# Kernel tuning notes

Hardware: AMD Instinct MI355X
Metric: run time of the kernel (lower is better)

The kernel has to match this reference:

```python
import jax, jax.numpy as jnp
import numpy as np

D, T, B = 128, 64, 512
EPS = 1e-5


def setup_inputs() -> dict:
    key = jax.random.key(0)
    k1, k2, k3, k4, k5 = jax.random.split(key, 5)
    inp = jax.random.normal(k1, (D, T, B), jnp.float32) * 0.1
    returns_partition = jax.random.normal(k2, (D, T, B), jnp.float32) * 0.01
    target = jax.random.normal(k3, (D,), jnp.float32) * 0.1
    hidden = jnp.zeros((D, 1, B), jnp.float32)  # forward arg (overwritten at t=0)
    # diagonally-dominant weight so the per-row denominators v[j,j] stay away from 0
    W = jnp.eye(D, dtype=jnp.float32) + 0.1 * jax.random.normal(k4, (D, D), jnp.float32)
    b = 0.1 * jax.random.normal(k5, (D,), jnp.float32)
    return {"input": inp, "target": target, "returns_partition": returns_partition,
            "hidden": hidden, "W": W, "b": b}


def _recurrence(h, v, absb, pi_bar):
    # h, pi_bar: [D, B]; v: [D, D] (row-normalized); absb: [D]
    d = h.shape[0]
    vd = jnp.diagonal(v)                                  # v[j, j], torch.matmul(vj, e_j)
    s = v @ (h - pi_bar)                                  # [D, B], s[j] = vj . (h - pi_bar)
    lam_p = (absb[:, None] - s) / vd[:, None]
    lam_m = (-absb[:, None] - s) / vd[:, None]
    delta = (jnp.where(s > absb[:, None], lam_p, 0.0)
             + jnp.where(s < -absb[:, None], lam_m, 0.0))  # [D, B]
    # hidden_new_j = h + delta[j] * e_j  =>  v @ (hidden_new_j - pi_bar) = s + v[:, j] (x) delta[j]
    snew = s[None, :, :] + v.T[:, :, None] * delta[:, None, :]      # [J, D, B]
    inside = (snew < absb[None, :, None] + EPS) & (snew > -absb[None, :, None] - EPS)
    # torch: judge_mat[j] = min over rows; then max over j  == any_j(all_k(...))
    judge_mat = jnp.any(jnp.all(inside, axis=1), axis=0).astype(h.dtype)  # [B]

    # sequential per-coordinate projection (order matters: row j uses updated state)
    def body(ht, j):
        sj = v[j] @ (ht - pi_bar)                          # [B]
        lp = (absb[j] - sj) / v[j, j]
        lm = (-absb[j] - sj) / v[j, j]
        dj = jnp.where(sj > absb[j], lp, 0.0) + jnp.where(sj < -absb[j], lm, 0.0)
        return ht.at[j].add(dj), None
    h_temp, _ = jax.lax.scan(body, h, jnp.arange(d))

    # 10-step bisection between pi_bar (feasible) and (1 - judge_mat) * h
    def bis(carry, _):
        h_in, h_out = carry
        h_m = h_in + (h_out - h_in) * 0.5
        sm = v @ (h_m - pi_bar)
        j = jnp.all((sm <= absb[:, None] + EPS) & (sm >= -absb[:, None] - EPS), axis=0)  # [B]
        return (jnp.where(j, h_m, h_in), jnp.where(j, h_out, h_m)), h_m
    h_out0 = (1.0 - judge_mat) * h
    _, h_ms = jax.lax.scan(bis, (pi_bar, h_out0), None, length=10)
    h_m = h_ms[-1]
    return judge_mat * h_temp + (1.0 - judge_mat) * h_m


def reference(input, target, returns_partition, hidden, W, b):
    d, t, bsz = input.shape
    norm = jnp.linalg.norm(W, axis=1, keepdims=True)
    v = W / jnp.maximum(norm, 1e-12)                      # F.normalize(W, p=2, dim=1)
    absb = jnp.abs(b)
    pi_bar = jnp.broadcast_to(target[:, None], (d, bsz))  # [D, B]

    h0 = input[:, 0, :]                                   # t = 0: hidden := input slice
    rs = jnp.moveaxis(returns_partition[:, :t - 1, :], 1, 0)  # [T-1, D, B]

    def step(h, r):
        adj = h * (1.0 + r) / (1.0 + jnp.sum(h * r, axis=0))
        hn = _recurrence(adj, v, absb, pi_bar)
        return hn, hn

    h_last, hs = jax.lax.scan(step, h0, rs)
    output = jnp.concatenate([h0[:, None, :], jnp.moveaxis(hs, 0, 1)], axis=1)  # [D, T, B]
    return output, h_last[:, None, :]
```

## Files before the change

kernel.cpp:

```cpp
#include <hip/hip_runtime.h>
#include <cstdint>

#define D 128
#define T 64
#define B 512
#define EPSF 1e-5f

__device__ __forceinline__ float lane_bcast(float x, int l) {
    return __int_as_float(__builtin_amdgcn_readlane(__float_as_int(x), l));
}

__device__ __forceinline__ float2 colpair(const float* csh, int j, int i2) {
    int f2 = j * 64 + (i2 ^ ((j & 7) << 1));
    return *(const float2*)(csh + 2 * f2);
}

__global__ __launch_bounds__(64) void prep_kernel(const float* __restrict__ W,
                                                  const float* __restrict__ b,
                                                  float* __restrict__ csw,
                                                  float* __restrict__ vd,
                                                  float* __restrict__ absb) {
    const int i = blockIdx.x;
    const int l = threadIdx.x;
    float w0 = W[i * D + l];
    float w1 = W[i * D + l + 64];
    float p = w0 * w0 + w1 * w1;
#pragma unroll
    for (int off = 32; off; off >>= 1) p += __shfl_xor(p, off);
    float norm = sqrtf(p);
    float scale = norm > 1e-12f ? norm : 1e-12f;
    float v0 = w0 / scale;
    float v1 = w1 / scale;
    const int i2 = i & 63, half = i >> 6;
    const int sw = (l & 7) << 1;
    csw[2 * (l * 64 + (i2 ^ sw)) + half] = v0;
    csw[2 * ((l + 64) * 64 + (i2 ^ sw)) + half] = v1;
    if (i < 64) { if (l == i) vd[i] = v0; }
    else        { if (l == i - 64) vd[i] = v1; }
    if (i == 0) {
        absb[l] = fabsf(b[l]);
        absb[l + 64] = fabsf(b[l + 64]);
    }
}

__global__ __launch_bounds__(128) void rnn_kernel(const float* __restrict__ input,
                                                  const float* __restrict__ target,
                                                  const float* __restrict__ returns,
                                                  const float* __restrict__ cswg,
                                                  const float* __restrict__ vdg,
                                                  const float* __restrict__ absbg,
                                                  float* __restrict__ out) {
    __shared__ float csh[D * D];
    __shared__ float s_sh[2][2 * 64];
    __shared__ float ae_sh[2 * 64];

    const int tid = threadIdx.x;
    const int w = tid >> 6;
    const int lane = tid & 63;
    const int b = blockIdx.x * 2 + w;
    const int rlo = lane, rhi = lane + 64;

    {
        const float4* src = (const float4*)cswg;
        float4* dst = (float4*)csh;
#pragma unroll
        for (int c = 0; c < 32; ++c) dst[c * 128 + tid] = src[c * 128 + tid];
    }

    const float tgt_lo = target[rlo], tgt_hi = target[rhi];
    const float a_lo = absbg[rlo], a_hi = absbg[rhi];
    const float aeps_lo = a_lo + EPSF, aeps_hi = a_hi + EPSF;
    const float vd_lo = vdg[rlo], vd_hi = vdg[rhi];
    const float rvd_lo = 1.0f / vd_lo, rvd_hi = 1.0f / vd_hi;

    if (w == 0) *(float2*)&ae_sh[2 * lane] = make_float2(aeps_lo, aeps_hi);
    __syncthreads();

    const char* colp[8];
#pragma unroll
    for (int c = 0; c < 8; ++c)
        colp[c] = (const char*)csh + 8 * (lane ^ (c << 1));

    float h_lo = input[rlo * T * B + b];
    float h_hi = input[rhi * T * B + b];
    out[rlo * T * B + b] = h_lo;
    out[rhi * T * B + b] = h_hi;

    float r_lo = returns[rlo * T * B + b];
    float r_hi = returns[rhi * T * B + b];

    for (int t = 1; t < T; ++t) {
        float num_lo = h_lo * (1.0f + r_lo);
        float num_hi = h_hi * (1.0f + r_hi);
        float p = h_lo * r_lo + h_hi * r_hi;
#pragma unroll
        for (int off = 32; off; off >>= 1) p += __shfl_xor(p, off);
        float den = 1.0f + p;
        float adj_lo = num_lo / den;
        float adj_hi = num_hi / den;

        if (t < T - 1) {
            r_lo = returns[rlo * T * B + t * B + b];
            r_hi = returns[rhi * T * B + t * B + b];
        }

        const float x_lo = adj_lo - tgt_lo;
        const float x_hi = adj_hi - tgt_hi;

        float a0 = 0, a1 = 0, a2 = 0, a3 = 0;
        float b0 = 0, b1 = 0, b2 = 0, b3 = 0;
#pragma unroll
        for (int k = 0; k < 128; ++k) {
            float2 cp = *(const float2*)(colp[k & 7] + k * 512);
            float xk = lane_bcast((k < 64) ? x_lo : x_hi, k & 63);
            switch (k & 3) {
                case 0: a0 = fmaf(cp.x, xk, a0); b0 = fmaf(cp.y, xk, b0); break;
                case 1: a1 = fmaf(cp.x, xk, a1); b1 = fmaf(cp.y, xk, b1); break;
                case 2: a2 = fmaf(cp.x, xk, a2); b2 = fmaf(cp.y, xk, b2); break;
                default: a3 = fmaf(cp.x, xk, a3); b3 = fmaf(cp.y, xk, b3); break;
            }
        }
        float s_lo = (a0 + a1) + (a2 + a3);
        float s_hi = (b0 + b1) + (b2 + b3);

        h_lo = adj_lo;
        h_hi = adj_hi;

        uint64_t mlo = __ballot(fabsf(s_lo) > a_lo);
        uint64_t mhi = __ballot(fabsf(s_hi) > a_hi);

        if ((mlo | mhi) != 0ull) {
            float dl = 0.0f, dh = 0.0f;
            if (s_lo > a_lo) dl = (a_lo - s_lo) / vd_lo;
            else if (s_lo < -a_lo) dl = (-a_lo - s_lo) / vd_lo;
            if (s_hi > a_hi) dh = (a_hi - s_hi) / vd_hi;
            else if (s_hi < -a_hi) dh = (-a_hi - s_hi) / vd_hi;

            int V = __popcll(mlo) + __popcll(mhi);
            bool judge = false;

            if (V <= 8) {
                bool in_lo = (s_lo < aeps_lo) && (s_lo > -aeps_lo);
                bool in_hi = (s_hi < aeps_hi) && (s_hi > -aeps_hi);
                judge = (__ballot(in_lo && in_hi) == ~0ull);
                if (!judge) {
                    uint64_t tml = mlo, tmh = mhi;
                    int jn[8];
                    float djs[8];
                    float2 cps[8];
#pragma unroll
                    for (int q = 0; q < 8; ++q) {
                        int j = -1;
                        if (tml) {
                            j = (int)__ffsll((unsigned long long)tml) - 1;
                            tml &= tml - 1;
                        } else if (tmh) {
                            j = 64 + (int)__ffsll((unsigned long long)tmh) - 1;
                            tmh &= tmh - 1;
                        }
                        jn[q] = j;
                        if (j >= 0) {
                            djs[q] = lane_bcast((j < 64) ? dl : dh, j & 63);
                            cps[q] = colpair(csh, j, lane);
                        }
                    }
#pragma unroll
                    for (int q = 0; q < 8; ++q) {
                        if (jn[q] >= 0 && !judge) {
                            float n_lo = fmaf(cps[q].x, djs[q], s_lo);
                            float n_hi = fmaf(cps[q].y, djs[q], s_hi);
                            bool pl = (n_lo < aeps_lo) && (n_lo > -aeps_lo);
                            bool ph = (n_hi < aeps_hi) && (n_hi > -aeps_hi);
                            if (__ballot(pl && ph) == ~0ull) judge = true;
                        }
                    }
                }
            } else {
                *(float2*)&s_sh[w][2 * lane] = make_float2(s_lo, s_hi);
                float m1 = -1.0f, m2 = -1.0f;
#pragma unroll
                for (int c = 0; c < 32; ++c) {
                    int f4 = lane * 32 + (c ^ (lane & 7));
                    float4 c1 = *(const float4*)(csh + 4 * f4);
                    float4 c2 = *(const float4*)(csh + 4 * f4 + 8192);
                    int i2a = (2 * c) ^ ((lane & 7) << 1);
                    float4 sv = *(const float4*)&s_sh[w][2 * i2a];
                    float4 ae = *(const float4*)&ae_sh[2 * i2a];
                    m1 = fmaxf(m1, fabsf(fmaf(c1.x, dl, sv.x)) - ae.x);
                    m1 = fmaxf(m1, fabsf(fmaf(c1.y, dl, sv.y)) - ae.y);
                    m1 = fmaxf(m1, fabsf(fmaf(c1.z, dl, sv.z)) - ae.z);
                    m1 = fmaxf(m1, fabsf(fmaf(c1.w, dl, sv.w)) - ae.w);
                    m2 = fmaxf(m2, fabsf(fmaf(c2.x, dh, sv.x)) - ae.x);
                    m2 = fmaxf(m2, fabsf(fmaf(c2.y, dh, sv.y)) - ae.y);
                    m2 = fmaxf(m2, fabsf(fmaf(c2.z, dh, sv.z)) - ae.z);
                    m2 = fmaxf(m2, fabsf(fmaf(c2.w, dh, sv.w)) - ae.w);
                }
                judge = ((__ballot(m1 < 0.0f) | __ballot(m2 < 0.0f)) != 0ull);
            }

            if (judge) {
                uint64_t rem_lo = ~0ull, rem_hi = ~0ull;
                while (true) {
                    uint64_t vl = __ballot(fabsf(s_lo) > a_lo) & rem_lo;
                    uint64_t vh = __ballot(fabsf(s_hi) > a_hi) & rem_hi;
                    if (!(vl | vh)) break;
                    int jq[4];
                    float2 cpq[4];
                    {
                        uint64_t tl = vl, th = vh;
#pragma unroll
                        for (int q = 0; q < 4; ++q) {
                            int j = -1;
                            if (tl) {
                                j = (int)__ffsll((unsigned long long)tl) - 1;
                                tl &= tl - 1;
                            } else if (th) {
                                j = 64 + (int)__ffsll((unsigned long long)th) - 1;
                                th &= th - 1;
                            }
                            jq[q] = j;
                            if (j >= 0) cpq[q] = colpair(csh, j, lane);
                        }
                    }
                    bool abort = false;
#pragma unroll
                    for (int q = 0; q < 4; ++q) {
                        if (abort || jq[q] < 0) continue;
                        uint64_t cl = __ballot(fabsf(s_lo) > a_lo) & rem_lo;
                        uint64_t ch = __ballot(fabsf(s_hi) > a_hi) & rem_hi;
                        int jl = cl ? (int)__ffsll((unsigned long long)cl) - 1
                                    : (ch ? 64 + (int)__ffsll((unsigned long long)ch) - 1 : -1);
                        if (jl < 0) { rem_lo = rem_hi = 0ull; abort = true; continue; }
                        if (jl < jq[q]) { abort = true; continue; }
                        if (jl > jq[q]) continue;
                        float tl2 = (s_lo > a_lo) ? (a_lo - s_lo)
                                   : ((s_lo < -a_lo) ? (-a_lo - s_lo) : 0.0f);
                        float th2 = (s_hi > a_hi) ? (a_hi - s_hi)
                                   : ((s_hi < -a_hi) ? (-a_hi - s_hi) : 0.0f);
                        float dj = lane_bcast((jq[q] < 64) ? tl2 * rvd_lo : th2 * rvd_hi,
                                              jq[q] & 63);
                        if (lane == (jq[q] & 63)) {
                            if (jq[q] < 64) h_lo += dj; else h_hi += dj;
                        }
                        s_lo = fmaf(cpq[q].x, dj, s_lo);
                        s_hi = fmaf(cpq[q].y, dj, s_hi);
                        if (jq[q] < 64) {
                            rem_lo = (jq[q] == 63) ? 0ull : (~0ull << (jq[q] + 1));
                        } else {
                            rem_lo = 0ull;
                            int sh = jq[q] - 64;
                            rem_hi = (sh == 63) ? 0ull : (~0ull << (sh + 1));
                        }
                    }
                    if (!(rem_lo | rem_hi)) break;
                }
            } else {
                float hin_lo = tgt_lo, hin_hi = tgt_hi;
                float sin_lo = 0.0f, sin_hi = 0.0f;
                float hout_lo = h_lo, hout_hi = h_hi;
                float sout_lo = s_lo, sout_hi = s_hi;
                float hm_lo = 0.0f, hm_hi = 0.0f;
#pragma unroll
                for (int it = 0; it < 10; ++it) {
                    hm_lo = hin_lo + (hout_lo - hin_lo) * 0.5f;
                    hm_hi = hin_hi + (hout_hi - hin_hi) * 0.5f;
                    float sm_lo = sin_lo + (sout_lo - sin_lo) * 0.5f;
                    float sm_hi = sin_hi + (sout_hi - sin_hi) * 0.5f;
                    bool pl = (sm_lo <= aeps_lo) && (sm_lo >= -aeps_lo);
                    bool ph = (sm_hi <= aeps_hi) && (sm_hi >= -aeps_hi);
                    bool inside = (__ballot(pl && ph) == ~0ull);
                    if (inside) {
                        hin_lo = hm_lo; hin_hi = hm_hi;
                        sin_lo = sm_lo; sin_hi = sm_hi;
                    } else {
                        hout_lo = hm_lo; hout_hi = hm_hi;
                        sout_lo = sm_lo; sout_hi = sm_hi;
                    }
                }
                h_lo = hm_lo;
                h_hi = hm_hi;
            }
        }

        out[rlo * T * B + t * B + b] = h_lo;
        out[rhi * T * B + t * B + b] = h_hi;
    }

    out[D * T * B + rlo * B + b] = h_lo;
    out[D * T * B + rhi * B + b] = h_hi;
}

extern "C" void kernel_launch(void* const* d_in, const int* in_sizes, int n_in,
                              void* d_out, int out_size, void* d_ws, size_t ws_size,
                              hipStream_t stream) {
    const float* input   = (const float*)d_in[0];
    const float* target  = (const float*)d_in[1];
    const float* returns = (const float*)d_in[2];
    const float* W = (const float*)d_in[4];
    const float* b = (const float*)d_in[5];
    float* out = (float*)d_out;

    float* csw  = (float*)d_ws;
    float* vd   = csw + D * D;
    float* absb = vd + D;

    prep_kernel<<<D, 64, 0, stream>>>(W, b, csw, vd, absb);
    rnn_kernel<<<B / 2, 128, 0, stream>>>(input, target, returns, csw, vd, absb, out);
}
```

Measured before the change: 235.5 us.

## Process two batch columns per wavefront to reuse each shared-memory weight load

Each 64-thread block now runs a single wavefront that handles two batch elements instead of one. Every float2 read of the normalized weight matrix from LDS therefore feeds FMAs for both samples, and the x vector is broadcast through LDS float4 reads rather than per-element readlane. Global loads and stores become float2 over the adjacent batch pair. The violation checks, sequential projection and bisection are duplicated per sample and run under shared control flow, so divergent paths may serialize. The block now holds 64KB of LDS for one wavefront, which halves the resident waves per CU.

```diff
diff --git a/kernel.cpp b/kernel.cpp
--- a/kernel.cpp
+++ b/kernel.cpp
@@ -43,28 +43,29 @@
     }
 }
 
-__global__ __launch_bounds__(128) void rnn_kernel(const float* __restrict__ input,
-                                                  const float* __restrict__ target,
-                                                  const float* __restrict__ returns,
-                                                  const float* __restrict__ cswg,
-                                                  const float* __restrict__ vdg,
-                                                  const float* __restrict__ absbg,
-                                                  float* __restrict__ out) {
+__global__ __launch_bounds__(64) void rnn_kernel(const float* __restrict__ input,
+                                                 const float* __restrict__ target,
+                                                 const float* __restrict__ returns,
+                                                 const float* __restrict__ cswg,
+                                                 const float* __restrict__ vdg,
+                                                 const float* __restrict__ absbg,
+                                                 float* __restrict__ out) {
     __shared__ float csh[D * D];
-    __shared__ float s_sh[2][2 * 64];
-    __shared__ float ae_sh[2 * 64];
-
-    const int tid = threadIdx.x;
-    const int w = tid >> 6;
-    const int lane = tid & 63;
-    const int b = blockIdx.x * 2 + w;
+    __shared__ __align__(16) float xsA[128];
+    __shared__ __align__(16) float xsB[128];
+    __shared__ __align__(16) float ssA[128];
+    __shared__ __align__(16) float ssB[128];
+    __shared__ __align__(16) float aes[128];
+
+    const int lane = threadIdx.x;
+    const int bA = blockIdx.x * 2;
     const int rlo = lane, rhi = lane + 64;
 
     {
         const float4* src = (const float4*)cswg;
         float4* dst = (float4*)csh;
 #pragma unroll
-        for (int c = 0; c < 32; ++c) dst[c * 128 + tid] = src[c * 128 + tid];
+        for (int c = 0; c < 64; ++c) dst[c * 64 + lane] = src[c * 64 + lane];
     }
 
     const float tgt_lo = target[rlo], tgt_hi = target[rhi];
@@ -72,222 +73,298 @@
     const float aeps_lo = a_lo + EPSF, aeps_hi = a_hi + EPSF;
     const float vd_lo = vdg[rlo], vd_hi = vdg[rhi];
     const float rvd_lo = 1.0f / vd_lo, rvd_hi = 1.0f / vd_hi;
-
-    if (w == 0) *(float2*)&ae_sh[2 * lane] = make_float2(aeps_lo, aeps_hi);
-    __syncthreads();
-
-    const char* colp[8];
-#pragma unroll
-    for (int c = 0; c < 8; ++c)
-        colp[c] = (const char*)csh + 8 * (lane ^ (c << 1));
-
-    float h_lo = input[rlo * T * B + b];
-    float h_hi = input[rhi * T * B + b];
-    out[rlo * T * B + b] = h_lo;
-    out[rhi * T * B + b] = h_hi;
-
-    float r_lo = returns[rlo * T * B + b];
-    float r_hi = returns[rhi * T * B + b];
+    *(float2*)&aes[2 * lane] = make_float2(aeps_lo, aeps_hi);
+
+    const char* cb[8];
+#pragma unroll
+    for (int c = 0; c < 8; ++c) cb[c] = (const char*)csh + 8 * (lane ^ (c << 1));
+
+    float2 hL = *(const float2*)&input[rlo * T * B + bA];
+    float2 hH = *(const float2*)&input[rhi * T * B + bA];
+    *(float2*)&out[rlo * T * B + bA] = hL;
+    *(float2*)&out[rhi * T * B + bA] = hH;
+    float hA_lo = hL.x, hB_lo = hL.y, hA_hi = hH.x, hB_hi = hH.y;
+
+    float2 r2L = *(const float2*)&returns[rlo * T * B + bA];
+    float2 r2H = *(const float2*)&returns[rhi * T * B + bA];
+    float rA_lo = r2L.x, rB_lo = r2L.y, rA_hi = r2H.x, rB_hi = r2H.y;
 
     for (int t = 1; t < T; ++t) {
-        float num_lo = h_lo * (1.0f + r_lo);
-        float num_hi = h_hi * (1.0f + r_hi);
-        float p = h_lo * r_lo + h_hi * r_hi;
-#pragma unroll
-        for (int off = 32; off; off >>= 1) p += __shfl_xor(p, off);
-        float den = 1.0f + p;
-        float adj_lo = num_lo / den;
-        float adj_hi = num_hi / den;
+        float pA = hA_lo * rA_lo + hA_hi * rA_hi;
+        float pB = hB_lo * rB_lo + hB_hi * rB_hi;
+#pragma unroll
+        for (int off = 32; off; off >>= 1) {
+            pA += __shfl_xor(pA, off);
+            pB += __shfl_xor(pB, off);
+        }
+        float rdA = 1.0f / (1.0f + pA);
+        float rdB = 1.0f / (1.0f + pB);
+        float adjA_lo = hA_lo * (1.0f + rA_lo) * rdA;
+        float adjA_hi = hA_hi * (1.0f + rA_hi) * rdA;
+        float adjB_lo = hB_lo * (1.0f + rB_lo) * rdB;
+        float adjB_hi = hB_hi * (1.0f + rB_hi) * rdB;
 
         if (t < T - 1) {
-            r_lo = returns[rlo * T * B + t * B + b];
-            r_hi = returns[rhi * T * B + t * B + b];
+            r2L = *(const float2*)&returns[rlo * T * B + t * B + bA];
+            r2H = *(const float2*)&returns[rhi * T * B + t * B + bA];
+            rA_lo = r2L.x; rB_lo = r2L.y; rA_hi = r2H.x; rB_hi = r2H.y;
         }
 
-        const float x_lo = adj_lo - tgt_lo;
-        const float x_hi = adj_hi - tgt_hi;
-
-        float a0 = 0, a1 = 0, a2 = 0, a3 = 0;
-        float b0 = 0, b1 = 0, b2 = 0, b3 = 0;
-#pragma unroll
-        for (int k = 0; k < 128; ++k) {
-            float2 cp = *(const float2*)(colp[k & 7] + k * 512);
-            float xk = lane_bcast((k < 64) ? x_lo : x_hi, k & 63);
-            switch (k & 3) {
-                case 0: a0 = fmaf(cp.x, xk, a0); b0 = fmaf(cp.y, xk, b0); break;
-                case 1: a1 = fmaf(cp.x, xk, a1); b1 = fmaf(cp.y, xk, b1); break;
-                case 2: a2 = fmaf(cp.x, xk, a2); b2 = fmaf(cp.y, xk, b2); break;
-                default: a3 = fmaf(cp.x, xk, a3); b3 = fmaf(cp.y, xk, b3); break;
+        float xA_lo = adjA_lo - tgt_lo, xA_hi = adjA_hi - tgt_hi;
+        float xB_lo = adjB_lo - tgt_lo, xB_hi = adjB_hi - tgt_hi;
+        xsA[lane] = xA_lo; xsA[64 + lane] = xA_hi;
+        xsB[lane] = xB_lo; xsB[64 + lane] = xB_hi;
+
+        float aL0 = 0, aL1 = 0, aH0 = 0, aH1 = 0;
+        float bL0 = 0, bL1 = 0, bH0 = 0, bH1 = 0;
+#pragma unroll
+        for (int m = 0; m < 32; ++m) {
+            float4 xA4 = *(const float4*)&xsA[4 * m];
+            float4 xB4 = *(const float4*)&xsB[4 * m];
+#pragma unroll
+            for (int e = 0; e < 4; ++e) {
+                const int k = 4 * m + e;
+                float2 vp = *(const float2*)(cb[k & 7] + k * 512);
+                float xa = (&xA4.x)[e], xb = (&xB4.x)[e];
+                if (e & 1) {
+                    aL1 = fmaf(vp.x, xa, aL1); aH1 = fmaf(vp.y, xa, aH1);
+                    bL1 = fmaf(vp.x, xb, bL1); bH1 = fmaf(vp.y, xb, bH1);
+                } else {
+                    aL0 = fmaf(vp.x, xa, aL0); aH0 = fmaf(vp.y, xa, aH0);
+                    bL0 = fmaf(vp.x, xb, bL0); bH0 = fmaf(vp.y, xb, bH0);
+                }
             }
         }
-        float s_lo = (a0 + a1) + (a2 + a3);
-        float s_hi = (b0 + b1) + (b2 + b3);
-
-        h_lo = adj_lo;
-        h_hi = adj_hi;
-
-        uint64_t mlo = __ballot(fabsf(s_lo) > a_lo);
-        uint64_t mhi = __ballot(fabsf(s_hi) > a_hi);
-
-        if ((mlo | mhi) != 0ull) {
-            float dl = 0.0f, dh = 0.0f;
-            if (s_lo > a_lo) dl = (a_lo - s_lo) / vd_lo;
-            else if (s_lo < -a_lo) dl = (-a_lo - s_lo) / vd_lo;
-            if (s_hi > a_hi) dh = (a_hi - s_hi) / vd_hi;
-            else if (s_hi < -a_hi) dh = (-a_hi - s_hi) / vd_hi;
-
-            int V = __popcll(mlo) + __popcll(mhi);
-            bool judge = false;
-
-            if (V <= 8) {
-                bool in_lo = (s_lo < aeps_lo) && (s_lo > -aeps_lo);
-                bool in_hi = (s_hi < aeps_hi) && (s_hi > -aeps_hi);
-                judge = (__ballot(in_lo && in_hi) == ~0ull);
-                if (!judge) {
-                    uint64_t tml = mlo, tmh = mhi;
-                    int jn[8];
-                    float djs[8];
-                    float2 cps[8];
-#pragma unroll
-                    for (int q = 0; q < 8; ++q) {
-                        int j = -1;
-                        if (tml) {
-                            j = (int)__ffsll((unsigned long long)tml) - 1;
-                            tml &= tml - 1;
-                        } else if (tmh) {
-                            j = 64 + (int)__ffsll((unsigned long long)tmh) - 1;
-                            tmh &= tmh - 1;
+        float sA_lo = aL0 + aL1, sA_hi = aH0 + aH1;
+        float sB_lo = bL0 + bL1, sB_hi = bH0 + bH1;
+
+        hA_lo = adjA_lo; hA_hi = adjA_hi;
+        hB_lo = adjB_lo; hB_hi = adjB_hi;
+
+        uint64_t mAlo = __ballot(fabsf(sA_lo) > a_lo);
+        uint64_t mAhi = __ballot(fabsf(sA_hi) > a_hi);
+        uint64_t mBlo = __ballot(fabsf(sB_lo) > a_lo);
+        uint64_t mBhi = __ballot(fabsf(sB_hi) > a_hi);
+        bool violA = (mAlo | mAhi) != 0ull;
+        bool violB = (mBlo | mBhi) != 0ull;
+
+        if (violA || violB) {
+            bool judgeA = true, judgeB = true;
+            bool needPJA = false, needPJB = false;
+            float dlA = 0, dhA = 0, dlB = 0, dhB = 0;
+
+            if (violA) {
+                if (sA_lo > a_lo) dlA = (a_lo - sA_lo) / vd_lo;
+                else if (sA_lo < -a_lo) dlA = (-a_lo - sA_lo) / vd_lo;
+                if (sA_hi > a_hi) dhA = (a_hi - sA_hi) / vd_hi;
+                else if (sA_hi < -a_hi) dhA = (-a_hi - sA_hi) / vd_hi;
+                int VA = __popcll(mAlo) + __popcll(mAhi);
+                if (VA <= 8) {
+                    bool in0 = (sA_lo < aeps_lo) && (sA_lo > -aeps_lo) &&
+                               (sA_hi < aeps_hi) && (sA_hi > -aeps_hi);
+                    judgeA = (__ballot(in0) == ~0ull);
+                    if (!judgeA) {
+                        uint64_t tml = mAlo, tmh = mAhi;
+                        unsigned bits = 0;
+#pragma unroll
+                        for (int q = 0; q < 8; ++q) {
+                            int j = -1;
+                            if (tml) { j = (int)__ffsll((unsigned long long)tml) - 1; tml &= tml - 1; }
+                            else if (tmh) { j = 64 + (int)__ffsll((unsigned long long)tmh) - 1; tmh &= tmh - 1; }
+                            if (j >= 0) {
+                                float dj = lane_bcast((j < 64) ? dlA : dhA, j & 63);
+                                float2 cp = colpair(csh, j, lane);
+                                float nlo = fmaf(cp.x, dj, sA_lo);
+                                float nhi = fmaf(cp.y, dj, sA_hi);
+                                bool ok = (nlo < aeps_lo) && (nlo > -aeps_lo) &&
+                                          (nhi < aeps_hi) && (nhi > -aeps_hi);
+                                bits |= ok ? (1u << q) : 0u;
+                            }
                         }
-                        jn[q] = j;
-                        if (j >= 0) {
-                            djs[q] = lane_bcast((j < 64) ? dl : dh, j & 63);
-                            cps[q] = colpair(csh, j, lane);
+#pragma unroll
+                        for (int off = 1; off < 64; off <<= 1)
+                            bits &= (unsigned)__shfl_xor((int)bits, off);
+                        judgeA = (bits != 0u);
+                    }
+                } else {
+                    needPJA = true;
+                }
+            }
+            if (violB) {
+                if (sB_lo > a_lo) dlB = (a_lo - sB_lo) / vd_lo;
+                else if (sB_lo < -a_lo) dlB = (-a_lo - sB_lo) / vd_lo;
+                if (sB_hi > a_hi) dhB = (a_hi - sB_hi) / vd_hi;
+                else if (sB_hi < -a_hi) dhB = (-a_hi - sB_hi) / vd_hi;
+                int VB = __popcll(mBlo) + __popcll(mBhi);
+                if (VB <= 8) {
+                    bool in0 = (sB_lo < aeps_lo) && (sB_lo > -aeps_lo) &&
+                               (sB_hi < aeps_hi) && (sB_hi > -aeps_hi);
+                    judgeB = (__ballot(in0) == ~0ull);
+                    if (!judgeB) {
+                        uint64_t tml = mBlo, tmh = mBhi;
+                        unsigned bits = 0;
+#pragma unroll
+                        for (int q = 0; q < 8; ++q) {
+                            int j = -1;
+                            if (tml) { j = (int)__ffsll((unsigned long long)tml) - 1; tml &= tml - 1; }
+                            else if (tmh) { j = 64 + (int)__ffsll((unsigned long long)tmh) - 1; tmh &= tmh - 1; }
+                            if (j >= 0) {
+                                float dj = lane_bcast((j < 64) ? dlB : dhB, j & 63);
+                                float2 cp = colpair(csh, j, lane);
+                                float nlo = fmaf(cp.x, dj, sB_lo);
+                                float nhi = fmaf(cp.y, dj, sB_hi);
+                                bool ok = (nlo < aeps_lo) && (nlo > -aeps_lo) &&
+                                          (nhi < aeps_hi) && (nhi > -aeps_hi);
+                                bits |= ok ? (1u << q) : 0u;
+                            }
                         }
-                    }
-#pragma unroll
-                    for (int q = 0; q < 8; ++q) {
-                        if (jn[q] >= 0 && !judge) {
-                            float n_lo = fmaf(cps[q].x, djs[q], s_lo);
-                            float n_hi = fmaf(cps[q].y, djs[q], s_hi);
-                            bool pl = (n_lo < aeps_lo) && (n_lo > -aeps_lo);
-                            bool ph = (n_hi < aeps_hi) && (n_hi > -aeps_hi);
-                            if (__ballot(pl && ph) == ~0ull) judge = true;
+#pragma unroll
+                        for (int off = 1; off < 64; off <<= 1)
+                            bits &= (unsigned)__shfl_xor((int)bits, off);
+                        judgeB = (bits != 0u);
+                    }
+                } else {
+                    needPJB = true;
+                }
+            }
+
+            if (needPJA || needPJB) {
+                if (needPJA) *(float2*)&ssA[2 * lane] = make_float2(sA_lo, sA_hi);
+                if (needPJB) *(float2*)&ssB[2 * lane] = make_float2(sB_lo, sB_hi);
+                float m1A = -1.0f, m2A = -1.0f, m1B = -1.0f, m2B = -1.0f;
+                const int jx = lane & 7;
+                const float* jbase = csh + 128 * lane;
+#pragma unroll
+                for (int c = 0; c < 32; ++c) {
+                    const float* pr = jbase + 4 * (c ^ jx);
+                    float4 c1 = *(const float4*)pr;
+                    float4 c2 = *(const float4*)(pr + 8192);
+                    float4 ae = *(const float4*)&aes[4 * c];
+                    if (needPJA) {
+                        float4 sv = *(const float4*)&ssA[4 * c];
+                        m1A = fmaxf(m1A, fabsf(fmaf(c1.x, dlA, sv.x)) - ae.x);
+                        m1A = fmaxf(m1A, fabsf(fmaf(c1.y, dlA, sv.y)) - ae.y);
+                        m1A = fmaxf(m1A, fabsf(fmaf(c1.z, dlA, sv.z)) - ae.z);
+                        m1A = fmaxf(m1A, fabsf(fmaf(c1.w, dlA, sv.w)) - ae.w);
+                        m2A = fmaxf(m2A, fabsf(fmaf(c2.x, dhA, sv.x)) - ae.x);
+                        m2A = fmaxf(m2A, fabsf(fmaf(c2.y, dhA, sv.y)) - ae.y);
+                        m2A = fmaxf(m2A, fabsf(fmaf(c2.z, dhA, sv.z)) - ae.z);
+                        m2A = fmaxf(m2A, fabsf(fmaf(c2.w, dhA, sv.w)) - ae.w);
+                    }
+                    if (needPJB) {
+                        float4 sv = *(const float4*)&ssB[4 * c];
+                        m1B = fmaxf(m1B, fabsf(fmaf(c1.x, dlB, sv.x)) - ae.x);
+                        m1B = fmaxf(m1B, fabsf(fmaf(c1.y, dlB, sv.y)) - ae.y);
+                        m1B = fmaxf(m1B, fabsf(fmaf(c1.z, dlB, sv.z)) - ae.z);
+                        m1B = fmaxf(m1B, fabsf(fmaf(c1.w, dlB, sv.w)) - ae.w);
+                        m2B = fmaxf(m2B, fabsf(fmaf(c2.x, dhB, sv.x)) - ae.x);
+                        m2B = fmaxf(m2B, fabsf(fmaf(c2.y, dhB, sv.y)) - ae.y);
+                        m2B = fmaxf(m2B, fabsf(fmaf(c2.z, dhB, sv.z)) - ae.z);
+                        m2B = fmaxf(m2B, fabsf(fmaf(c2.w, dhB, sv.w)) - ae.w);
+                    }
+                }
+                if (needPJA)
+                    judgeA = ((__ballot(m1A < 0.0f) | __ballot(m2A < 0.0f)) != 0ull);
+                if (needPJB)
+                    judgeB = ((__ballot(m1B < 0.0f) | __ballot(m2B < 0.0f)) != 0ull);
+            }
+
+            bool swA = violA && judgeA, swB = violB && judgeB;
+            bool biA = violA && !judgeA, biB = violB && !judgeB;
+
+            if (swA || swB) {
+                uint64_t remAlo = swA ? ~0ull : 0ull, remAhi = swA ? ~0ull : 0ull;
+                uint64_t remBlo = swB ? ~0ull : 0ull, remBhi = swB ? ~0ull : 0ull;
+                while (true) {
+                    uint64_t vAl = __ballot(fabsf(sA_lo) > a_lo) & remAlo;
+                    uint64_t vAh = __ballot(fabsf(sA_hi) > a_hi) & remAhi;
+                    uint64_t vBl = __ballot(fabsf(sB_lo) > a_lo) & remBlo;
+                    uint64_t vBh = __ballot(fabsf(sB_hi) > a_hi) & remBhi;
+                    int jA = -1, jB = -1;
+                    if (vAl) jA = (int)__ffsll((unsigned long long)vAl) - 1;
+                    else if (vAh) jA = 64 + (int)__ffsll((unsigned long long)vAh) - 1;
+                    if (vBl) jB = (int)__ffsll((unsigned long long)vBl) - 1;
+                    else if (vBh) jB = 64 + (int)__ffsll((unsigned long long)vBh) - 1;
+                    if (jA < 0 && jB < 0) break;
+                    float2 cA = make_float2(0.0f, 0.0f), cB = make_float2(0.0f, 0.0f);
+                    if (jA >= 0) cA = colpair(csh, jA, lane);
+                    if (jB >= 0) cB = colpair(csh, jB, lane);
+                    if (jA >= 0) {
+                        if (jA < 64) remAlo = (jA == 63) ? 0ull : (~0ull << (jA + 1));
+                        else { remAlo = 0ull; int s = jA - 64;
+                               remAhi = (s == 63) ? 0ull : (~0ull << (s + 1)); }
+                        float d1 = (sA_lo > a_lo) ? (a_lo - sA_lo) * rvd_lo
+                                 : ((sA_lo < -a_lo) ? (-a_lo - sA_lo) * rvd_lo : 0.0f);
+                        float d2 = (sA_hi > a_hi) ? (a_hi - sA_hi) * rvd_hi
+                                 : ((sA_hi < -a_hi) ? (-a_hi - sA_hi) * rvd_hi : 0.0f);
+                        float dj = lane_bcast((jA < 64) ? d1 : d2, jA & 63);
+                        if (lane == (jA & 63)) {
+                            if (jA < 64) hA_lo += dj; else hA_hi += dj;
                         }
-                    }
-                }
-            } else {
-                *(float2*)&s_sh[w][2 * lane] = make_float2(s_lo, s_hi);
-                float m1 = -1.0f, m2 = -1.0f;
-#pragma unroll
-                for (int c = 0; c < 32; ++c) {
-                    int f4 = lane * 32 + (c ^ (lane & 7));
-                    float4 c1 = *(const float4*)(csh + 4 * f4);
-                    float4 c2 = *(const float4*)(csh + 4 * f4 + 8192);
-                    int i2a = (2 * c) ^ ((lane & 7) << 1);
-                    float4 sv = *(const float4*)&s_sh[w][2 * i2a];
-                    float4 ae = *(const float4*)&ae_sh[2 * i2a];
-                    m1 = fmaxf(m1, fabsf(fmaf(c1.x, dl, sv.x)) - ae.x);
-                    m1 = fmaxf(m1, fabsf(fmaf(c1.y, dl, sv.y)) - ae.y);
-                    m1 = fmaxf(m1, fabsf(fmaf(c1.z, dl, sv.z)) - ae.z);
-                    m1 = fmaxf(m1, fabsf(fmaf(c1.w, dl, sv.w)) - ae.w);
-                    m2 = fmaxf(m2, fabsf(fmaf(c2.x, dh, sv.x)) - ae.x);
-                    m2 = fmaxf(m2, fabsf(fmaf(c2.y, dh, sv.y)) - ae.y);
-                    m2 = fmaxf(m2, fabsf(fmaf(c2.z, dh, sv.z)) - ae.z);
-                    m2 = fmaxf(m2, fabsf(fmaf(c2.w, dh, sv.w)) - ae.w);
-                }
-                judge = ((__ballot(m1 < 0.0f) | __ballot(m2 < 0.0f)) != 0ull);
-            }
-
-            if (judge) {
-                uint64_t rem_lo = ~0ull, rem_hi = ~0ull;
-                while (true) {
-                    uint64_t vl = __ballot(fabsf(s_lo) > a_lo) & rem_lo;
-                    uint64_t vh = __ballot(fabsf(s_hi) > a_hi) & rem_hi;
-                    if (!(vl | vh)) break;
-                    int jq[4];
-                    float2 cpq[4];
-                    {
-                        uint64_t tl = vl, th = vh;
-#pragma unroll
-                        for (int q = 0; q < 4; ++q) {
-                            int j = -1;
-                            if (tl) {
-                                j = (int)__ffsll((unsigned long long)tl) - 1;
-                                tl &= tl - 1;
-                            } else if (th) {
-                                j = 64 + (int)__ffsll((unsigned long long)th) - 1;
-                                th &= th - 1;
-                            }
-                            jq[q] = j;
-                            if (j >= 0) cpq[q] = colpair(csh, j, lane);
+                        sA_lo = fmaf(cA.x, dj, sA_lo);
+                        sA_hi = fmaf(cA.y, dj, sA_hi);
+                    }
+                    if (jB >= 0) {
+                        if (jB < 64) remBlo = (jB == 63) ? 0ull : (~0ull << (jB + 1));
+                        else { remBlo = 0ull; int s = jB - 64;
+                               remBhi = (s == 63) ? 0ull : (~0ull << (s + 1)); }
+                        float d1 = (sB_lo > a_lo) ? (a_lo - sB_lo) * rvd_lo
+                                 : ((sB_lo < -a_lo) ? (-a_lo - sB_lo) * rvd_lo : 0.0f);
+                        float d2 = (sB_hi > a_hi) ? (a_hi - sB_hi) * rvd_hi
+                                 : ((sB_hi < -a_hi) ? (-a_hi - sB_hi) * rvd_hi : 0.0f);
+                        float dj = lane_bcast((jB < 64) ? d1 : d2, jB & 63);
+                        if (lane == (jB & 63)) {
+                            if (jB < 64) hB_lo += dj; else hB_hi += dj;
                         }
-                    }
-                    bool abort = false;
-#pragma unroll
-                    for (int q = 0; q < 4; ++q) {
-                        if (abort || jq[q] < 0) continue;
-                        uint64_t cl = __ballot(fabsf(s_lo) > a_lo) & rem_lo;
-                        uint64_t ch = __ballot(fabsf(s_hi) > a_hi) & rem_hi;
-                        int jl = cl ? (int)__ffsll((unsigned long long)cl) - 1
-                                    : (ch ? 64 + (int)__ffsll((unsigned long long)ch) - 1 : -1);
-                        if (jl < 0) { rem_lo = rem_hi = 0ull; abort = true; continue; }
-                        if (jl < jq[q]) { abort = true; continue; }
-                        if (jl > jq[q]) continue;
-                        float tl2 = (s_lo > a_lo) ? (a_lo - s_lo)
-                                   : ((s_lo < -a_lo) ? (-a_lo - s_lo) : 0.0f);
-                        float th2 = (s_hi > a_hi) ? (a_hi - s_hi)
-                                   : ((s_hi < -a_hi) ? (-a_hi - s_hi) : 0.0f);
-                        float dj = lane_bcast((jq[q] < 64) ? tl2 * rvd_lo : th2 * rvd_hi,
-                                              jq[q] & 63);
-                        if (lane == (jq[q] & 63)) {
-                            if (jq[q] < 64) h_lo += dj; else h_hi += dj;
-                        }
-                        s_lo = fmaf(cpq[q].x, dj, s_lo);
-                        s_hi = fmaf(cpq[q].y, dj, s_hi);
-                        if (jq[q] < 64) {
-                            rem_lo = (jq[q] == 63) ? 0ull : (~0ull << (jq[q] + 1));
-                        } else {
-                            rem_lo = 0ull;
-                            int sh = jq[q] - 64;
-                            rem_hi = (sh == 63) ? 0ull : (~0ull << (sh + 1));
-                        }
-                    }
-                    if (!(rem_lo | rem_hi)) break;
-                }
-            } else {
-                float hin_lo = tgt_lo, hin_hi = tgt_hi;
-                float sin_lo = 0.0f, sin_hi = 0.0f;
-                float hout_lo = h_lo, hout_hi = h_hi;
-                float sout_lo = s_lo, sout_hi = s_hi;
-                float hm_lo = 0.0f, hm_hi = 0.0f;
+                        sB_lo = fmaf(cB.x, dj, sB_lo);
+                        sB_hi = fmaf(cB.y, dj, sB_hi);
+                    }
+                }
+            }
+
+            if (biA || biB) {
+                float hinAlo = tgt_lo, hinAhi = tgt_hi, sinAlo = 0, sinAhi = 0;
+                float houtAlo = hA_lo, houtAhi = hA_hi, soutAlo = sA_lo, soutAhi = sA_hi;
+                float hmAlo = 0, hmAhi = 0;
+                float hinBlo = tgt_lo, hinBhi = tgt_hi, sinBlo = 0, sinBhi = 0;
+                float houtBlo = hB_lo, houtBhi = hB_hi, soutBlo = sB_lo, soutBhi = sB_hi;
+                float hmBlo = 0, hmBhi = 0;
 #pragma unroll
                 for (int it = 0; it < 10; ++it) {
-                    hm_lo = hin_lo + (hout_lo - hin_lo) * 0.5f;
-                    hm_hi = hin_hi + (hout_hi - hin_hi) * 0.5f;
-                    float sm_lo = sin_lo + (sout_lo - sin_lo) * 0.5f;
-                    float sm_hi = sin_hi + (sout_hi - sin_hi) * 0.5f;
-                    bool pl = (sm_lo <= aeps_lo) && (sm_lo >= -aeps_lo);
-                    bool ph = (sm_hi <= aeps_hi) && (sm_hi >= -aeps_hi);
-                    bool inside = (__ballot(pl && ph) == ~0ull);
-                    if (inside) {
-                        hin_lo = hm_lo; hin_hi = hm_hi;
-                        sin_lo = sm_lo; sin_hi = sm_hi;
-                    } else {
-                        hout_lo = hm_lo; hout_hi = hm_hi;
-                        sout_lo = sm_lo; sout_hi = sm_hi;
-                    }
-                }
-                h_lo = hm_lo;
-                h_hi = hm_hi;
+                    if (biA) {
+                        hmAlo = hinAlo + (houtAlo - hinAlo) * 0.5f;
+                        hmAhi = hinAhi + (houtAhi - hinAhi) * 0.5f;
+                        float smlo = sinAlo + (soutAlo - sinAlo) * 0.5f;
+                        float smhi = sinAhi + (soutAhi - sinAhi) * 0.5f;
+                        bool ok = (smlo <= aeps_lo) && (smlo >= -aeps_lo) &&
+                                  (smhi <= aeps_hi) && (smhi >= -aeps_hi);
+                        bool inside = (__ballot(ok) == ~0ull);
+                        if (inside) { hinAlo = hmAlo; hinAhi = hmAhi; sinAlo = smlo; sinAhi = smhi; }
+                        else { houtAlo = hmAlo; houtAhi = hmAhi; soutAlo = smlo; soutAhi = smhi; }
+                    }
+                    if (biB) {
+                        hmBlo = hinBlo + (houtBlo - hinBlo) * 0.5f;
+                        hmBhi = hinBhi + (houtBhi - hinBhi) * 0.5f;
+                        float smlo = sinBlo + (soutBlo - sinBlo) * 0.5f;
+                        float smhi = sinBhi + (soutBhi - sinBhi) * 0.5f;
+                        bool ok = (smlo <= aeps_lo) && (smlo >= -aeps_lo) &&
+                                  (smhi <= aeps_hi) && (smhi >= -aeps_hi);
+                        bool inside = (__ballot(ok) == ~0ull);
+                        if (inside) { hinBlo = hmBlo; hinBhi = hmBhi; sinBlo = smlo; sinBhi = smhi; }
+                        else { houtBlo = hmBlo; houtBhi = hmBhi; soutBlo = smlo; soutBhi = smhi; }
+                    }
+                }
+                if (biA) { hA_lo = hmAlo; hA_hi = hmAhi; }
+                if (biB) { hB_lo = hmBlo; hB_hi = hmBhi; }
             }
         }
 
-        out[rlo * T * B + t * B + b] = h_lo;
-        out[rhi * T * B + t * B + b] = h_hi;
+        *(float2*)&out[rlo * T * B + t * B + bA] = make_float2(hA_lo, hB_lo);
+        *(float2*)&out[rhi * T * B + t * B + bA] = make_float2(hA_hi, hB_hi);
     }
 
-    out[D * T * B + rlo * B + b] = h_lo;
-    out[D * T * B + rhi * B + b] = h_hi;
+    *(float2*)&out[D * T * B + rlo * B + bA] = make_float2(hA_lo, hB_lo);
+    *(float2*)&out[D * T * B + rhi * B + bA] = make_float2(hA_hi, hB_hi);
 }
 
 extern "C" void kernel_launch(void* const* d_in, const int* in_sizes, int n_in,
@@ -305,5 +382,5 @@
     float* absb = vd + D;
 
     prep_kernel<<<D, 64, 0, stream>>>(W, b, csw, vd, absb);
-    rnn_kernel<<<B / 2, 128, 0, stream>>>(input, target, returns, csw, vd, absb, out);
-}
+    rnn_kernel<<<B / 2, 64, 0, stream>>>(input, target, returns, csw, vd, absb, out);
+}
```

After: 385.4 us. +63.7%, slower.
